# Performance work log

Hardware: AMD Instinct MI355X
Metric: run time of the kernel (lower is better)

## Reference

```python
import jax, jax.numpy as jnp
import numpy as np

B, T, DIM, HEADS = 4, 2048, 1024, 16
D_K = DIM // HEADS


def setup_inputs() -> dict:
    key = jax.random.key(0)
    ks = jax.random.split(key, 5)
    x = jax.random.normal(ks[0], (B, T, DIM), dtype=jnp.float32)
    # nn.Linear params: weight [out, in], bias [out]
    w_qkv = jax.random.normal(ks[1], (3 * DIM, DIM), dtype=jnp.float32) / np.sqrt(DIM)
    b_qkv = jax.random.normal(ks[2], (3 * DIM,), dtype=jnp.float32) * 0.02
    w_out = jax.random.normal(ks[3], (DIM, DIM), dtype=jnp.float32) / np.sqrt(DIM)
    b_out = jax.random.normal(ks[4], (DIM,), dtype=jnp.float32) * 0.02
    # causal mask, broadcast over batch and heads: [1, 1, T, T]
    mask = jnp.tril(jnp.ones((T, T), dtype=jnp.int32))[None, None]
    return {"x": x, "w_qkv": w_qkv, "b_qkv": b_qkv, "w_out": w_out, "b_out": b_out, "mask": mask}


def reference(x, w_qkv, b_qkv, w_out, b_out, mask):
    Bb, Tt, D = x.shape
    # fused QKV projection: [B,T,3D] -> [3,B,H,T,d_k]
    qkv = (x @ w_qkv.T + b_qkv).reshape(Bb, Tt, 3, HEADS, D_K).transpose(2, 0, 3, 1, 4)
    q, k, v = qkv[0], qkv[1], qkv[2]
    scores = jnp.einsum("bhqd,bhkd->bhqk", q, k) / jnp.sqrt(jnp.float32(D_K))
    scores = jnp.where(mask == 0, -jnp.inf, scores)
    attn = jax.nn.softmax(scores, axis=-1)  # [B,H,T,T]
    context = jnp.einsum("bhqk,bhkd->bhqd", attn, v)
    context = context.transpose(0, 2, 1, 3).reshape(Bb, Tt, D)
    return context @ w_out.T + b_out
```

## Files before the change

### kernel.cpp

```cpp
#include <hip/hip_runtime.h>

typedef unsigned short ushort_t;
typedef __bf16 bf16x8 __attribute__((ext_vector_type(8)));
typedef float f32x4 __attribute__((ext_vector_type(4)));

#define BB 4
#define TT 2048
#define DIMD 1024
#define NH 16
#define DK 64
#define MROWS (BB * TT)
#define NQKV (3 * DIMD)

__device__ __forceinline__ ushort_t f2b(float f) {
  __bf16 h = (__bf16)f;
  union { __bf16 h; ushort_t u; } c; c.h = h; return c.u;
}
__device__ __forceinline__ float fexp2(float x) {
  float r;
  asm("v_exp_f32 %0, %1" : "=v"(r) : "v"(x));
  return r;
}

__device__ __forceinline__ void gload_lds16(const void* g, void* l) {
  __builtin_amdgcn_global_load_lds(
      (const __attribute__((address_space(1))) void*)g,
      (__attribute__((address_space(3))) void*)l,
      16, 0, 0);
}

__global__ __launch_bounds__(256) void cast_f32_bf16(
    const float* __restrict__ in, ushort_t* __restrict__ out, int n)
{
  const int i = (blockIdx.x * 256 + threadIdx.x) * 8;
  if (i >= n) return;
  float4 a = *(const float4*)(in + i);
  float4 b = *(const float4*)(in + i + 4);
  ushort_t o[8];
  o[0] = f2b(a.x); o[1] = f2b(a.y); o[2] = f2b(a.z); o[3] = f2b(a.w);
  o[4] = f2b(b.x); o[5] = f2b(b.y); o[6] = f2b(b.z); o[7] = f2b(b.w);
  *(uint4*)(out + i) = *(const uint4*)o;
}

template <bool OUT_F32>
__global__ __launch_bounds__(512, 4) void gemm_bt_pipe(
    const ushort_t* __restrict__ A, const ushort_t* __restrict__ W,
    const float* __restrict__ bias, void* __restrict__ Cp,
    int M, int N, int K)
{
  __shared__ __align__(16) ushort_t As[3][128 * 32];
  __shared__ __align__(16) ushort_t Bs[3][256 * 32];

  const int tid = threadIdx.x;
  const int wave = tid >> 6, lane = tid & 63;
  const int x = blockIdx.x & 7, j = blockIdx.x >> 3;
  const int bm = (x << 3) | (j & 7);
  const int bn = j >> 3;
  const int row0 = bm << 7, col0 = bn << 8;
  const int wm = (wave >> 2) << 6;
  const int wn = (wave & 3) << 6;
  const int fr = lane & 15;
  const int g  = lane >> 4;
  const int g4 = g << 2;
  const int csw = (g ^ (fr >> 2)) << 3;

  const int srow = lane >> 2;
  const int scol = ((lane & 3) ^ ((lane >> 4) & 3)) << 3;
  const int lbase = wave << 9;

  const ushort_t* Ag  = A + (size_t)(row0 + (wave << 4) + srow) * K + scol;
  const ushort_t* Wg0 = W + (size_t)(col0 + (wave << 4) + srow) * K + scol;
  const ushort_t* Wg1 = Wg0 + (size_t)128 * K;

#define STAGE_P(kt, buf)                                                      \
  {                                                                           \
    const size_t _k = (size_t)(kt) << 5;                                      \
    gload_lds16(Ag + _k,  &As[buf][lbase]);                                   \
    gload_lds16(Wg0 + _k, &Bs[buf][lbase]);                                   \
    gload_lds16(Wg1 + _k, &Bs[buf][4096 + lbase]);                            \
  }

  const int NT = K >> 5;
  STAGE_P(0, 0);
  STAGE_P(1, 1);

  f32x4 acc[4][4] = {};
  int cr = 0, st = 2;

  for (int t = 0; t < NT; ++t) {
    if (t + 1 < NT) asm volatile("s_waitcnt vmcnt(3)" ::: "memory");
    else            asm volatile("s_waitcnt vmcnt(0)" ::: "memory");
    __builtin_amdgcn_s_barrier();

    const ushort_t* as_ = As[cr];
    const ushort_t* bs_ = Bs[cr];
    bf16x8 af0 = *(const bf16x8*)&as_[(wm +      fr) * 32 + csw];
    bf16x8 af1 = *(const bf16x8*)&as_[(wm + 16 + fr) * 32 + csw];
    bf16x8 bw0 = *(const bf16x8*)&bs_[(wn +      fr) * 32 + csw];
    bf16x8 bw1 = *(const bf16x8*)&bs_[(wn + 16 + fr) * 32 + csw];
    bf16x8 bw2 = *(const bf16x8*)&bs_[(wn + 32 + fr) * 32 + csw];
    bf16x8 bw3 = *(const bf16x8*)&bs_[(wn + 48 + fr) * 32 + csw];
    if (t + 2 < NT) STAGE_P(t + 2, st);
    asm volatile("s_waitcnt lgkmcnt(0)" ::: "memory");
    __builtin_amdgcn_sched_barrier(0);
    __builtin_amdgcn_s_setprio(1);
    acc[0][0] = __builtin_amdgcn_mfma_f32_16x16x32_bf16(af0, bw0, acc[0][0], 0, 0, 0);
    acc[0][1] = __builtin_amdgcn_mfma_f32_16x16x32_bf16(af0, bw1, acc[0][1], 0, 0, 0);
    acc[0][2] = __builtin_amdgcn_mfma_f32_16x16x32_bf16(af0, bw2, acc[0][2], 0, 0, 0);
    acc[0][3] = __builtin_amdgcn_mfma_f32_16x16x32_bf16(af0, bw3, acc[0][3], 0, 0, 0);
    acc[1][0] = __builtin_amdgcn_mfma_f32_16x16x32_bf16(af1, bw0, acc[1][0], 0, 0, 0);
    acc[1][1] = __builtin_amdgcn_mfma_f32_16x16x32_bf16(af1, bw1, acc[1][1], 0, 0, 0);
    acc[1][2] = __builtin_amdgcn_mfma_f32_16x16x32_bf16(af1, bw2, acc[1][2], 0, 0, 0);
    acc[1][3] = __builtin_amdgcn_mfma_f32_16x16x32_bf16(af1, bw3, acc[1][3], 0, 0, 0);
    __builtin_amdgcn_s_setprio(0);

    bf16x8 af2 = *(const bf16x8*)&as_[(wm + 32 + fr) * 32 + csw];
    bf16x8 af3 = *(const bf16x8*)&as_[(wm + 48 + fr) * 32 + csw];
    asm volatile("s_waitcnt lgkmcnt(0)" ::: "memory");
    __builtin_amdgcn_sched_barrier(0);
    __builtin_amdgcn_s_setprio(1);
    acc[2][0] = __builtin_amdgcn_mfma_f32_16x16x32_bf16(af2, bw0, acc[2][0], 0, 0, 0);
    acc[2][1] = __builtin_amdgcn_mfma_f32_16x16x32_bf16(af2, bw1, acc[2][1], 0, 0, 0);
    acc[2][2] = __builtin_amdgcn_mfma_f32_16x16x32_bf16(af2, bw2, acc[2][2], 0, 0, 0);
    acc[2][3] = __builtin_amdgcn_mfma_f32_16x16x32_bf16(af2, bw3, acc[2][3], 0, 0, 0);
    acc[3][0] = __builtin_amdgcn_mfma_f32_16x16x32_bf16(af3, bw0, acc[3][0], 0, 0, 0);
    acc[3][1] = __builtin_amdgcn_mfma_f32_16x16x32_bf16(af3, bw1, acc[3][1], 0, 0, 0);
    acc[3][2] = __builtin_amdgcn_mfma_f32_16x16x32_bf16(af3, bw2, acc[3][2], 0, 0, 0);
    acc[3][3] = __builtin_amdgcn_mfma_f32_16x16x32_bf16(af3, bw3, acc[3][3], 0, 0, 0);
    __builtin_amdgcn_s_setprio(0);

    ++cr; if (cr == 3) cr = 0;
    ++st; if (st == 3) st = 0;
  }
#undef STAGE_P

#pragma unroll
  for (int jj = 0; jj < 4; ++jj) {
    const int col = col0 + wn + (jj << 4) + fr;
    const float bv = bias[col];
#pragma unroll
    for (int i = 0; i < 4; ++i)
#pragma unroll
      for (int r = 0; r < 4; ++r) {
        const size_t row = (size_t)(row0 + wm + (i << 4) + g4 + r);
        if constexpr (OUT_F32)
          ((float*)Cp)[row * (size_t)N + col] = acc[i][jj][r] + bv;
        else
          ((ushort_t*)Cp)[row * (size_t)N + col] = f2b(acc[i][jj][r] + bv);
      }
  }
}

template <bool OUT_F32>
__global__ __launch_bounds__(256) void gemm_bt_bias(
    const ushort_t* __restrict__ A, const ushort_t* __restrict__ W,
    const float* __restrict__ bias, void* __restrict__ Cp,
    int M, int N, int K)
{
  __shared__ __align__(16) ushort_t As[128 * 32];
  __shared__ __align__(16) ushort_t Bs[128 * 32];

  const int tid = threadIdx.x;
  const int wave = tid >> 6, lane = tid & 63;
  const int tiles_n = N >> 7;
  const int bm = blockIdx.x / tiles_n, bn = blockIdx.x % tiles_n;
  const int row0 = bm << 7, col0 = bn << 7;
  const int wm = (wave >> 1) << 6;
  const int wn = (wave & 1) << 6;
  const int fr = lane & 15;
  const int fk = (lane >> 4) << 3;
  const int g4 = (lane >> 4) << 2;

  const int sr = lane >> 2;
  const int csw = fk ^ (((fr >> 1) & 3) << 3);

  f32x4 acc[4][4] = {};

  for (int k0 = 0; k0 < K; k0 += 32) {
    __syncthreads();
#pragma unroll
    for (int p = 0; p < 2; ++p) {
      const int e = (wave << 9) + (p << 11);
      const int r = (e >> 5) + sr;
      const int c = ((lane & 3) << 3) ^ (((r >> 1) & 3) << 3);
      gload_lds16(A + (size_t)(row0 + r) * K + (k0 + c), As + e);
      gload_lds16(W + (size_t)(col0 + r) * K + (k0 + c), Bs + e);
    }
    __syncthreads();

    bf16x8 af[4], bw[4];
#pragma unroll
    for (int i = 0; i < 4; ++i) {
      af[i] = *(const bf16x8*)&As[(wm + (i << 4) + fr) * 32 + csw];
      bw[i] = *(const bf16x8*)&Bs[(wn + (i << 4) + fr) * 32 + csw];
    }
#pragma unroll
    for (int mi = 0; mi < 4; ++mi)
#pragma unroll
      for (int ni = 0; ni < 4; ++ni)
        acc[mi][ni] = __builtin_amdgcn_mfma_f32_16x16x32_bf16(af[mi], bw[ni], acc[mi][ni], 0, 0, 0);
  }

#pragma unroll
  for (int ni = 0; ni < 4; ++ni) {
    const int col = col0 + wn + (ni << 4) + fr;
    const float bv = bias[col];
#pragma unroll
    for (int mi = 0; mi < 4; ++mi)
#pragma unroll
      for (int r = 0; r < 4; ++r) {
        const size_t row = (size_t)(row0 + wm + (mi << 4) + g4 + r);
        if constexpr (OUT_F32)
          ((float*)Cp)[row * (size_t)N + col] = acc[mi][ni][r] + bv;
        else
          ((ushort_t*)Cp)[row * (size_t)N + col] = f2b(acc[mi][ni][r] + bv);
      }
  }
}

#define C1 0.18033688011112042f
__global__ __launch_bounds__(512, 4) void attn_fused(
    const ushort_t* __restrict__ qkv, ushort_t* __restrict__ ctx)
{
  __shared__ __align__(16) ushort_t Ks[2][64 * 64];
  __shared__ __align__(16) ushort_t U[12288];
  ushort_t* const Vt = U;
  ushort_t* const Ps = U + 4096;
  ushort_t* const Qs = U;

  const int tid = threadIdx.x, wave = tid >> 6, lane = tid & 63;
  const int fr = lane & 15;
  const int g  = lane >> 4;
  const int fk = g << 3;
  const int g4 = g << 2;

  const int bid = blockIdx.x;
  const int qt  = 15 - ((bid >> 3) & 15);
  const int G   = (bid & 7) | ((bid >> 7) << 3);
  const int h   = G & 15;
  const int b   = G >> 4;

  const int srl = lane >> 3;
  const int scc = ((lane & 7) ^ srl) << 3;
  const int vr  = tid >> 3;
  const int vc  = (tid & 7) << 3;
  const int rsw = (fr & 7) << 3;

  const ushort_t* Kg = qkv + (size_t)b * TT * NQKV + DIMD + h * DK;
  const ushort_t* Vg = qkv + (size_t)b * TT * NQKV + 2 * DIMD + h * DK;

  const int ktmax = 2 * qt + 1;
  const int diag  = 2 * qt + (wave >> 2);
  const size_t qrow0 = (size_t)b * TT + (size_t)qt * 128;

  const ushort_t* Qg = qkv + qrow0 * NQKV + h * DK;
  uint4 va = *(const uint4*)(Vg + (size_t)vr * NQKV + vc);
#pragma unroll
  for (int pp = 0; pp < 2; ++pp) {
    const int e  = (wave << 9) + (pp << 12);
    const int rr = (e >> 6) + srl;
    gload_lds16(Qg + (size_t)rr * NQKV + scc, Qs + e);
  }
  {
    const int e  = wave << 9;
    const int rr = (wave << 3) + srl;
    gload_lds16(Kg + (size_t)rr * NQKV + scc, Ks[0] + e);
  }
  asm volatile("s_waitcnt vmcnt(0)" ::: "memory");
  __syncthreads();

  bf16x8 aqr[2];
#pragma unroll
  for (int ks = 0; ks < 2; ++ks)
    aqr[ks] = *(const bf16x8*)&Qs[((wave << 4) + fr) * 64 + (((ks << 5) + fk) ^ rsw)];
  __syncthreads();

  const int qrow = (qt << 7) + (wave << 4) + fr;
  float mrow = -1e30f, lrow = 0.f;
  f32x4 oacc[4] = {};
  int cur = 0;

  for (int kt = 0; kt <= ktmax; ++kt) {
    {
      __align__(16) ushort_t tmp[8];
      *(uint4*)tmp = va;
#pragma unroll
      for (int jj = 0; jj < 8; ++jj) {
        const int d  = vc + jj;
        const int hh = (d & 7) ^ ((d >> 3) & 7);
        Vt[d * 64 + (vr ^ (hh << 3))] = tmp[jj];
      }
    }
    if (kt < ktmax) {
      const size_t krow = (size_t)(kt + 1) << 6;
      const int e  = wave << 9;
      const int rr = (wave << 3) + srl;
      gload_lds16(Kg + (krow + rr) * NQKV + scc, Ks[cur ^ 1] + e);
      va = *(const uint4*)(Vg + (krow + vr) * NQKV + vc);
    }
    asm volatile("s_waitcnt lgkmcnt(0)" ::: "memory");
    __builtin_amdgcn_s_barrier();

    if (kt <= diag) {
      f32x4 s[4] = {};
      __builtin_amdgcn_s_setprio(1);
#pragma unroll
      for (int ks = 0; ks < 2; ++ks)
#pragma unroll
        for (int ni = 0; ni < 4; ++ni) {
          const bf16x8 bk = *(const bf16x8*)&Ks[cur][((ni << 4) + fr) * 64 + (((ks << 5) + fk) ^ rsw)];
          s[ni] = __builtin_amdgcn_mfma_f32_16x16x32_bf16(bk, aqr[ks], s[ni], 0, 0, 0);
        }
      __builtin_amdgcn_s_setprio(0);

      if (kt == diag) {
        const int kb = kt << 6;
#pragma unroll
        for (int ni = 0; ni < 4; ++ni)
#pragma unroll
          for (int r = 0; r < 4; ++r) {
            const int kc = kb + (ni << 4) + g4 + r;
            if (kc > qrow) s[ni][r] = -1e30f;
          }
      }

      float rm = -1e30f;
#pragma unroll
      for (int ni = 0; ni < 4; ++ni) {
        const float m01 = fmaxf(s[ni][0], s[ni][1]);
        const float m23 = fmaxf(s[ni][2], s[ni][3]);
        rm = fmaxf(rm, fmaxf(m01, m23));
      }
      rm = fmaxf(rm, __shfl_xor(rm, 16, 64));
      rm = fmaxf(rm, __shfl_xor(rm, 32, 64));

      if (__any(rm > mrow + 64.f)) {
        const float mn = fmaxf(mrow, rm);
        const float corr = fexp2((mrow - mn) * C1);
        mrow = mn;
        lrow *= corr;
#pragma unroll
        for (int ni = 0; ni < 4; ++ni) oacc[ni] *= corr;
      }
      const float nm2 = -mrow * C1;
      float rs = 0.f;
#pragma unroll
      for (int ni = 0; ni < 4; ++ni)
#pragma unroll
        for (int r = 0; r < 4; ++r) {
          const float pe = fexp2(fmaf(s[ni][r], C1, nm2));
          s[ni][r] = pe;
          rs += pe;
        }
      rs += __shfl_xor(rs, 16, 64);
      rs += __shfl_xor(rs, 32, 64);
      lrow += rs;

#pragma unroll
      for (int ni = 0; ni < 4; ++ni) {
        ushort_t o4[4];
#pragma unroll
        for (int r = 0; r < 4; ++r) o4[r] = f2b(s[ni][r]);
        *(uint2*)&Ps[(wave << 10) + fr * 64 + (((ni << 4) + g4) ^ rsw)] = *(const uint2*)o4;
      }
      asm volatile("s_waitcnt lgkmcnt(0)" ::: "memory");
      __builtin_amdgcn_sched_barrier(0);

      __builtin_amdgcn_s_setprio(1);
#pragma unroll
      for (int ks = 0; ks < 2; ++ks) {
        const bf16x8 ap = *(const bf16x8*)&Ps[(wave << 10) + fr * 64 + (((ks << 5) + fk) ^ rsw)];
#pragma unroll
        for (int ni = 0; ni < 4; ++ni) {
          const int hh = (fr & 7) ^ ((2 * ni + (fr >> 3)) & 7);
          const bf16x8 bv = *(const bf16x8*)&Vt[((ni << 4) + fr) * 64 + (((ks << 5) + fk) ^ (hh << 3))];
          oacc[ni] = __builtin_amdgcn_mfma_f32_16x16x32_bf16(bv, ap, oacc[ni], 0, 0, 0);
        }
      }
      __builtin_amdgcn_s_setprio(0);
    }

    if (kt < ktmax) {
      asm volatile("s_waitcnt vmcnt(0)" ::: "memory");
      __syncthreads();
    }
    cur ^= 1;
  }

  const float inv = 1.f / lrow;
  ushort_t* crow = ctx + (qrow0 + (wave << 4) + fr) * DIMD + h * DK;
#pragma unroll
  for (int ni = 0; ni < 4; ++ni) {
    ushort_t o4[4];
#pragma unroll
    for (int r = 0; r < 4; ++r) o4[r] = f2b(oacc[ni][r] * inv);
    *(uint2*)&crow[(ni << 4) + g4] = *(const uint2*)o4;
  }
}

extern "C" void kernel_launch(void* const* d_in, const int* in_sizes, int n_in,
                              void* d_out, int out_size, void* d_ws, size_t ws_size,
                              hipStream_t stream) {
  const float* x     = (const float*)d_in[0];
  const float* w_qkv = (const float*)d_in[1];
  const float* b_qkv = (const float*)d_in[2];
  const float* w_out = (const float*)d_in[3];
  const float* b_out = (const float*)d_in[4];

  const size_t need = 36u * 1024 * 1024 * sizeof(ushort_t);
  if (ws_size < need) return;

  ushort_t* qkv = (ushort_t*)d_ws;
  ushort_t* xb  = qkv + (size_t)MROWS * NQKV;
  ushort_t* wqb = xb  + (size_t)MROWS * DIMD;
  ushort_t* wob = wqb + (size_t)NQKV * DIMD;
  ushort_t* ctx = xb;
  float*    out = (float*)d_out;

  cast_f32_bf16<<<dim3(MROWS * DIMD / 2048), dim3(256), 0, stream>>>(x, xb, MROWS * DIMD);
  cast_f32_bf16<<<dim3(NQKV * DIMD / 2048), dim3(256), 0, stream>>>(w_qkv, wqb, NQKV * DIMD);
  cast_f32_bf16<<<dim3(DIMD * DIMD / 2048), dim3(256), 0, stream>>>(w_out, wob, DIMD * DIMD);
  gemm_bt_pipe<false><<<dim3((MROWS / 128) * (NQKV / 256)), dim3(512), 0, stream>>>(
      xb, wqb, b_qkv, (void*)qkv, MROWS, NQKV, DIMD);
  attn_fused<<<dim3(BB * NH * 16), dim3(512), 0, stream>>>(qkv, ctx);
  gemm_bt_bias<true><<<dim3((MROWS / 128) * (DIMD / 128)), dim3(256), 0, stream>>>(
      ctx, wob, b_out, (void*)out, MROWS, DIMD, DIMD);
}
```

Before: 204.0 us.

## Pair causal query tiles per block with 4-wave attention blocks

The attention kernel now uses 256-thread blocks, each handling two 64-row query tiles (bq and 31-bq), so every block does the same amount of causal work. The old version used 128-row tiles in 8-wave blocks, where half the waves idled on the diagonal tile. Each thread now loads twice as much K/V per step, and the LDS footprint shrinks. The cost is fewer waves per block to hide latency, plus a serial second pass that repeats the Q/K prologue.

Result: faster. 186.9 us (-8.4%).

```diff
diff --git a/kernel.cpp b/kernel.cpp
--- a/kernel.cpp
+++ b/kernel.cpp
@@ -219,11 +219,11 @@
 }
 
 #define C1 0.18033688011112042f
-__global__ __launch_bounds__(512, 4) void attn_fused(
+__global__ __launch_bounds__(256, 4) void attn_fused(
     const ushort_t* __restrict__ qkv, ushort_t* __restrict__ ctx)
 {
   __shared__ __align__(16) ushort_t Ks[2][64 * 64];
-  __shared__ __align__(16) ushort_t U[12288];
+  __shared__ __align__(16) ushort_t U[8192];
   ushort_t* const Vt = U;
   ushort_t* const Ps = U + 4096;
   ushort_t* const Qs = U;
@@ -235,73 +235,78 @@
   const int g4 = g << 2;
 
   const int bid = blockIdx.x;
-  const int qt  = 15 - ((bid >> 3) & 15);
+  const int bq  = (bid >> 3) & 15;
   const int G   = (bid & 7) | ((bid >> 7) << 3);
   const int h   = G & 15;
   const int b   = G >> 4;
 
   const int srl = lane >> 3;
   const int scc = ((lane & 7) ^ srl) << 3;
-  const int vr  = tid >> 3;
-  const int vc  = (tid & 7) << 3;
+  const int vr  = tid >> 2;
+  const int vc  = (tid & 3) << 4;
   const int rsw = (fr & 7) << 3;
 
   const ushort_t* Kg = qkv + (size_t)b * TT * NQKV + DIMD + h * DK;
   const ushort_t* Vg = qkv + (size_t)b * TT * NQKV + 2 * DIMD + h * DK;
 
-  const int ktmax = 2 * qt + 1;
-  const int diag  = 2 * qt + (wave >> 2);
-  const size_t qrow0 = (size_t)b * TT + (size_t)qt * 128;
-
-  const ushort_t* Qg = qkv + qrow0 * NQKV + h * DK;
-  uint4 va = *(const uint4*)(Vg + (size_t)vr * NQKV + vc);
-#pragma unroll
-  for (int pp = 0; pp < 2; ++pp) {
-    const int e  = (wave << 9) + (pp << 12);
-    const int rr = (e >> 6) + srl;
-    gload_lds16(Qg + (size_t)rr * NQKV + scc, Qs + e);
-  }
-  {
-    const int e  = wave << 9;
-    const int rr = (wave << 3) + srl;
-    gload_lds16(Kg + (size_t)rr * NQKV + scc, Ks[0] + e);
-  }
-  asm volatile("s_waitcnt vmcnt(0)" ::: "memory");
-  __syncthreads();
-
-  bf16x8 aqr[2];
-#pragma unroll
-  for (int ks = 0; ks < 2; ++ks)
-    aqr[ks] = *(const bf16x8*)&Qs[((wave << 4) + fr) * 64 + (((ks << 5) + fk) ^ rsw)];
-  __syncthreads();
-
-  const int qrow = (qt << 7) + (wave << 4) + fr;
-  float mrow = -1e30f, lrow = 0.f;
-  f32x4 oacc[4] = {};
-  int cur = 0;
-
-  for (int kt = 0; kt <= ktmax; ++kt) {
-    {
-      __align__(16) ushort_t tmp[8];
-      *(uint4*)tmp = va;
-#pragma unroll
-      for (int jj = 0; jj < 8; ++jj) {
-        const int d  = vc + jj;
-        const int hh = (d & 7) ^ ((d >> 3) & 7);
-        Vt[d * 64 + (vr ^ (hh << 3))] = tmp[jj];
-      }
+#pragma unroll 1
+  for (int t = 0; t < 2; ++t) {
+    const int qt = t ? (31 - bq) : bq;
+    const int ktmax = qt;
+    const size_t qrow0 = (size_t)b * TT + (size_t)qt * 64;
+
+    __syncthreads();
+
+    const ushort_t* Qg = qkv + qrow0 * NQKV + h * DK;
+    uint4 va = *(const uint4*)(Vg + (size_t)vr * NQKV + vc);
+    uint4 vb = *(const uint4*)(Vg + (size_t)vr * NQKV + vc + 8);
+#pragma unroll
+    for (int p = 0; p < 2; ++p) {
+      const int e  = (wave << 10) + (p << 9);
+      const int rr = (e >> 6) + srl;
+      gload_lds16(Qg + (size_t)rr * NQKV + scc, Qs + e);
+      gload_lds16(Kg + (size_t)rr * NQKV + scc, Ks[0] + e);
     }
-    if (kt < ktmax) {
-      const size_t krow = (size_t)(kt + 1) << 6;
-      const int e  = wave << 9;
-      const int rr = (wave << 3) + srl;
-      gload_lds16(Kg + (krow + rr) * NQKV + scc, Ks[cur ^ 1] + e);
-      va = *(const uint4*)(Vg + (krow + vr) * NQKV + vc);
-    }
-    asm volatile("s_waitcnt lgkmcnt(0)" ::: "memory");
-    __builtin_amdgcn_s_barrier();
-
-    if (kt <= diag) {
+    asm volatile("s_waitcnt vmcnt(0)" ::: "memory");
+    __syncthreads();
+
+    bf16x8 aqr[2];
+#pragma unroll
+    for (int ks = 0; ks < 2; ++ks)
+      aqr[ks] = *(const bf16x8*)&Qs[((wave << 4) + fr) * 64 + (((ks << 5) + fk) ^ rsw)];
+    __syncthreads();
+
+    const int qrow = (qt << 6) + (wave << 4) + fr;
+    float mrow = -1e30f, lrow = 0.f;
+    f32x4 oacc[4] = {};
+    int cur = 0;
+
+    for (int kt = 0; kt <= ktmax; ++kt) {
+      {
+        __align__(16) ushort_t tmp[16];
+        *(uint4*)&tmp[0] = va;
+        *(uint4*)&tmp[8] = vb;
+#pragma unroll
+        for (int jj = 0; jj < 16; ++jj) {
+          const int d  = vc + jj;
+          const int hh = (d & 7) ^ ((d >> 3) & 7);
+          Vt[d * 64 + (vr ^ (hh << 3))] = tmp[jj];
+        }
+      }
+      if (kt < ktmax) {
+        const size_t krow = (size_t)(kt + 1) << 6;
+#pragma unroll
+        for (int p = 0; p < 2; ++p) {
+          const int e  = (wave << 10) + (p << 9);
+          const int rr = (e >> 6) + srl;
+          gload_lds16(Kg + (krow + rr) * NQKV + scc, Ks[cur ^ 1] + e);
+        }
+        va = *(const uint4*)(Vg + (krow + vr) * NQKV + vc);
+        vb = *(const uint4*)(Vg + (krow + vr) * NQKV + vc + 8);
+      }
+      asm volatile("s_waitcnt lgkmcnt(0)" ::: "memory");
+      __builtin_amdgcn_s_barrier();
+
       f32x4 s[4] = {};
       __builtin_amdgcn_s_setprio(1);
 #pragma unroll
@@ -313,7 +318,7 @@
         }
       __builtin_amdgcn_s_setprio(0);
 
-      if (kt == diag) {
+      if (kt == ktmax) {
         const int kb = kt << 6;
 #pragma unroll
         for (int ni = 0; ni < 4; ++ni)
@@ -378,23 +383,23 @@
         }
       }
       __builtin_amdgcn_s_setprio(0);
+
+      if (kt < ktmax) {
+        asm volatile("s_waitcnt vmcnt(0)" ::: "memory");
+        __syncthreads();
+      }
+      cur ^= 1;
     }
 
-    if (kt < ktmax) {
-      asm volatile("s_waitcnt vmcnt(0)" ::: "memory");
-      __syncthreads();
+    const float inv = 1.f / lrow;
+    ushort_t* crow = ctx + (qrow0 + (wave << 4) + fr) * DIMD + h * DK;
+#pragma unroll
+    for (int ni = 0; ni < 4; ++ni) {
+      ushort_t o4[4];
+#pragma unroll
+      for (int r = 0; r < 4; ++r) o4[r] = f2b(oacc[ni][r] * inv);
+      *(uint2*)&crow[(ni << 4) + g4] = *(const uint2*)o4;
     }
-    cur ^= 1;
-  }
-
-  const float inv = 1.f / lrow;
-  ushort_t* crow = ctx + (qrow0 + (wave << 4) + fr) * DIMD + h * DK;
-#pragma unroll
-  for (int ni = 0; ni < 4; ++ni) {
-    ushort_t o4[4];
-#pragma unroll
-    for (int r = 0; r < 4; ++r) o4[r] = f2b(oacc[ni][r] * inv);
-    *(uint2*)&crow[(ni << 4) + g4] = *(const uint2*)o4;
   }
 }
 
@@ -422,7 +427,7 @@
   cast_f32_bf16<<<dim3(DIMD * DIMD / 2048), dim3(256), 0, stream>>>(w_out, wob, DIMD * DIMD);
   gemm_bt_pipe<false><<<dim3((MROWS / 128) * (NQKV / 256)), dim3(512), 0, stream>>>(
       xb, wqb, b_qkv, (void*)qkv, MROWS, NQKV, DIMD);
-  attn_fused<<<dim3(BB * NH * 16), dim3(512), 0, stream>>>(qkv, ctx);
+  attn_fused<<<dim3(BB * NH * 16), dim3(256), 0, stream>>>(qkv, ctx);
   gemm_bt_bias<true><<<dim3((MROWS / 128) * (DIMD / 128)), dim3(256), 0, stream>>>(
       ctx, wob, b_out, (void*)out, MROWS, DIMD, DIMD);
 }
```
